# Kernel optimization log

Hardware: AMD Instinct MI355X
Metric: run time of the kernel (lower is better)

Reference implementation:

```python
import jax, jax.numpy as jnp
import numpy as np

VOCAB = 32000
EMBED = 512
CTX = 256
HID = 1024
MAX_SEQ = 1024
B, S = 4, 1024


def setup_inputs() -> dict:
    key = jax.random.key(0)
    ks = jax.random.split(key, 12)
    std = 0.02
    inp = {
        "input_ids": jax.random.randint(ks[0], (B, S), 0, VOCAB, dtype=jnp.int64 if jax.config.jax_enable_x64 else jnp.int32),
        "tok_emb": jax.random.normal(ks[1], (VOCAB, EMBED), jnp.float32) * std,
        "pos_emb": jax.random.normal(ks[2], (MAX_SEQ, EMBED), jnp.float32) * std,
        "W0": jax.random.normal(ks[3], (HID, EMBED + CTX), jnp.float32) * std,
        "b0": jnp.zeros((HID,), jnp.float32),
        "W1": jax.random.normal(ks[4], (HID, HID), jnp.float32) * std,
        "b1": jnp.zeros((HID,), jnp.float32),
        "Wout": jax.random.normal(ks[5], (VOCAB, HID), jnp.float32) * std,
        "bout": jnp.zeros((VOCAB,), jnp.float32),
        "Wc": jax.random.normal(ks[6], (CTX, HID), jnp.float32) * std,
        "bc": jnp.zeros((CTX,), jnp.float32),
    }
    return inp


def reference(input_ids, tok_emb, pos_emb, W0, b0, W1, b1, Wout, bout, Wc, bc):
    # embeddings: [B, S, E]
    seq_len = input_ids.shape[1]
    x = tok_emb[input_ids] + pos_emb[:seq_len][None, :, :]
    ctx0 = jnp.zeros((input_ids.shape[0], Wc.shape[0]), x.dtype)

    def step(ctx, xt):
        # xt: [B, E]; ctx: [B, C]
        h = jax.nn.relu(jnp.concatenate([xt, ctx], axis=-1) @ W0.T + b0)  # layer 0
        h = jax.nn.relu(h @ W1.T + b1)                                    # layer 1
        logits = h @ Wout.T + bout                                        # [B, V]
        new_ctx = ctx + h @ Wc.T + bc
        return new_ctx, (logits, ctx)  # trajectory stores ctx BEFORE update, as in torch

    _, (logits, traj) = jax.lax.scan(step, ctx0, jnp.swapaxes(x, 0, 1))
    # logits: [S, B, V] -> [B, S, V]; traj: [S, B, C] -> [B, S, C]
    return jnp.swapaxes(logits, 0, 1), jnp.swapaxes(traj, 0, 1)
```

## Files before the change

kernel.cpp:

```cpp
#include <hip/hip_runtime.h>
#include <stdint.h>

#define VOCABN 32000
#define EMBEDN 512
#define CTXN   256
#define HIDN   1024
#define BN     4
#define SN     1024
#define MTOT   (BN*SN)

typedef __attribute__((ext_vector_type(8))) short short8;
typedef __attribute__((ext_vector_type(4))) float f32x4;

__device__ __forceinline__ ushort f2bf(float f) {
    uint x = __float_as_uint(f);
    uint r = (x + 0x7FFFu + ((x >> 16) & 1u)) >> 16;
    return (ushort)r;
}
__device__ __forceinline__ float bf2f(ushort h) { return __uint_as_float((uint)h << 16); }
__device__ __forceinline__ float bflo(uint p) { return __uint_as_float(p << 16); }
__device__ __forceinline__ float bfhi(uint p) { return __uint_as_float(p & 0xFFFF0000u); }

__global__ __launch_bounds__(256) void embed_kernel(
    const int* __restrict__ ids, const float* __restrict__ tok,
    const float* __restrict__ pos, ushort* __restrict__ X)
{
    int i = blockIdx.x * 256 + threadIdx.x;
    int m = i >> 7;
    int e4 = (i & 127) * 4;
    int id = ids[m];
    int tp = m & 1023;
    float4 a = *(const float4*)(tok + (size_t)id * EMBEDN + e4);
    float4 b = *(const float4*)(pos + (size_t)tp * EMBEDN + e4);
    ushort4 r;
    r.x = f2bf(a.x + b.x); r.y = f2bf(a.y + b.y);
    r.z = f2bf(a.z + b.z); r.w = f2bf(a.w + b.w);
    *(ushort4*)(X + (size_t)m * EMBEDN + e4) = r;
}

__global__ __launch_bounds__(256) void gemm_bt(
    const ushort* __restrict__ A, const float* __restrict__ B,
    const float* __restrict__ bias, float* __restrict__ C,
    int M, int N, int K, int ldb)
{
    __shared__ ushort As[128 * 40];
    __shared__ ushort Bs[128 * 40];

    const int tid = threadIdx.x;
    const int bm = blockIdx.y, bn = blockIdx.x;
    const int wid = tid >> 6, lane = tid & 63;
    const int wm = wid & 1, wn = wid >> 1;
    const int r15 = lane & 15, kq = lane >> 4;

    f32x4 acc[4][4] = {};

    const int row = tid >> 1, seg = (tid & 1) * 16;
    const ushort* asrc = A + (size_t)(bm * 128 + row) * K + seg;
    const float*  bsrc = B + (size_t)(bn * 128 + row) * ldb + seg;
    ushort* adst = &As[row * 40 + seg];
    ushort* bdst = &Bs[row * 40 + seg];

    for (int k0 = 0; k0 < K; k0 += 32) {
        uint4 a0 = *(const uint4*)(asrc + k0);
        uint4 a1 = *(const uint4*)(asrc + k0 + 8);
        float4 f0 = *(const float4*)(bsrc + k0);
        float4 f1 = *(const float4*)(bsrc + k0 + 4);
        float4 f2 = *(const float4*)(bsrc + k0 + 8);
        float4 f3 = *(const float4*)(bsrc + k0 + 12);
        uint4 p0, p1;
        p0.x = (uint)f2bf(f0.x) | ((uint)f2bf(f0.y) << 16);
        p0.y = (uint)f2bf(f0.z) | ((uint)f2bf(f0.w) << 16);
        p0.z = (uint)f2bf(f1.x) | ((uint)f2bf(f1.y) << 16);
        p0.w = (uint)f2bf(f1.z) | ((uint)f2bf(f1.w) << 16);
        p1.x = (uint)f2bf(f2.x) | ((uint)f2bf(f2.y) << 16);
        p1.y = (uint)f2bf(f2.z) | ((uint)f2bf(f2.w) << 16);
        p1.z = (uint)f2bf(f3.x) | ((uint)f2bf(f3.y) << 16);
        p1.w = (uint)f2bf(f3.z) | ((uint)f2bf(f3.w) << 16);
        *(uint4*)adst = a0;
        *(uint4*)(adst + 8) = a1;
        *(uint4*)bdst = p0;
        *(uint4*)(bdst + 8) = p1;
        __syncthreads();

        short8 af[4], bfv[4];
        #pragma unroll
        for (int mt = 0; mt < 4; ++mt)
            af[mt] = *(const short8*)&As[(wm * 64 + mt * 16 + r15) * 40 + kq * 8];
        #pragma unroll
        for (int nt = 0; nt < 4; ++nt)
            bfv[nt] = *(const short8*)&Bs[(wn * 64 + nt * 16 + r15) * 40 + kq * 8];
        #pragma unroll
        for (int mt = 0; mt < 4; ++mt)
            #pragma unroll
            for (int nt = 0; nt < 4; ++nt)
                acc[mt][nt] = __builtin_amdgcn_mfma_f32_16x16x32_bf16(
                    af[mt], bfv[nt], acc[mt][nt], 0, 0, 0);
        __syncthreads();
    }

    #pragma unroll
    for (int mt = 0; mt < 4; ++mt) {
        #pragma unroll
        for (int nt = 0; nt < 4; ++nt) {
            int n = bn * 128 + wn * 64 + nt * 16 + r15;
            float bv = bias[n];
            #pragma unroll
            for (int i = 0; i < 4; ++i) {
                int m = bm * 128 + wm * 64 + mt * 16 + kq * 4 + i;
                C[(size_t)m * N + n] = acc[mt][nt][i] + bv;
            }
        }
    }
}

__global__ __launch_bounds__(256) void mk_kernel(
    const float* __restrict__ W0, const float* __restrict__ Wc,
    float* __restrict__ M)
{
    __shared__ float w0r[4][256];
    const int tid = threadIdx.x;
    const int i0 = blockIdx.x * 4;
    for (int idx = tid; idx < 1024; idx += 256) {
        int r = idx >> 8, c = idx & 255;
        w0r[r][c] = W0[(size_t)(i0 + r) * 768 + 512 + c];
    }
    __syncthreads();
    for (int rep = 0; rep < 4; ++rep) {
        int j = rep * 256 + tid;
        float a0 = 0, a1 = 0, a2 = 0, a3 = 0;
        for (int c = 0; c < 256; ++c) {
            float wv = Wc[(size_t)c * 1024 + j];
            a0 += w0r[0][c] * wv; a1 += w0r[1][c] * wv;
            a2 += w0r[2][c] * wv; a3 += w0r[3][c] * wv;
        }
        M[(size_t)(i0 + 0) * 1024 + j] = a0;
        M[(size_t)(i0 + 1) * 1024 + j] = a1;
        M[(size_t)(i0 + 2) * 1024 + j] = a2;
        M[(size_t)(i0 + 3) * 1024 + j] = a3;
    }
}

__device__ __forceinline__ void gbar(uint* bar, int& ep) {
    __syncthreads();
    if (threadIdx.x == 0) {
        __hip_atomic_fetch_add(bar, 1u, __ATOMIC_RELEASE, __HIP_MEMORY_SCOPE_AGENT);
        uint tgt = (uint)(++ep) * 64u;
        while (__hip_atomic_load(bar, __ATOMIC_ACQUIRE, __HIP_MEMORY_SCOPE_AGENT) < tgt) {}
    }
    __syncthreads();
}

__global__ __launch_bounds__(256) void rec_kernel(
    const float* __restrict__ W0, const float* __restrict__ W1g,
    const float* __restrict__ b1g, const float* __restrict__ bcg,
    const float* __restrict__ Mg,
    uint* h0hi, uint* h0lo, uint* h1hi, uint* h1lo, uint* bar,
    const float* __restrict__ u_g, ushort* __restrict__ Hout)
{
    extern __shared__ char smem[];
    ushort* W1f_hi = (ushort*)(smem);
    ushort* W1f_lo = (ushort*)(smem + 32768);
    ushort* Mf_hi  = (ushort*)(smem + 65536);
    ushort* Mf_lo  = (ushort*)(smem + 98304);
    uint*   st_hi  = (uint*)(smem + 131072);
    uint*   st_lo  = (uint*)(smem + 139392);
    float*  red    = (float*)(smem + 147712);
    float*  hloc   = (float*)(smem + 148736);
    float*  a_s    = (float*)(smem + 148992);
    float*  b1s    = (float*)(smem + 149248);
    float*  ds_    = (float*)(smem + 149312);

    const int wg = blockIdx.x, tid = threadIdx.x;
    const int wv = tid >> 6, lane = tid & 63;

    for (int idx = tid; idx < 16384; idx += 256) {
        int j = idx & 7, ln = (idx >> 3) & 63, ks = idx >> 9;
        int m = ln & 15, kq = ln >> 4;
        int k = ks * 32 + kq * 8 + j;
        float w1 = W1g[(size_t)(wg * 16 + m) * 1024 + k];
        ushort h = f2bf(w1);
        W1f_hi[idx] = h;
        W1f_lo[idx] = f2bf(w1 - bf2f(h));
        float mm = Mg[(size_t)(wg * 16 + m) * 1024 + k];
        ushort mh = f2bf(mm);
        Mf_hi[idx] = mh;
        Mf_lo[idx] = f2bf(mm - bf2f(mh));
    }
    if (tid < 16) {
        b1s[tid] = b1g[wg * 16 + tid];
        float acc = 0.f;
        for (int c = 0; c < 256; ++c)
            acc += W0[(size_t)(wg * 16 + tid) * 768 + 512 + c] * bcg[c];
        ds_[tid] = acc;
    }
    if (tid < 64) a_s[tid] = 0.f;

    float u_reg = 0.f;
    if (tid < 64)
        u_reg = u_g[(size_t)((tid >> 4) * 1024 + 0) * 1024 + wg * 16 + (tid & 15)];
    __syncthreads();

    int ep = 0;
    for (int t = 0; t < SN; ++t) {
        if (tid < 64) hloc[tid] = fmaxf(u_reg + a_s[tid], 0.f);
        __syncthreads();
        if (tid < 32) {
            int s = tid >> 3, j = tid & 7;
            float x0 = hloc[s * 16 + 2 * j], x1 = hloc[s * 16 + 2 * j + 1];
            ushort p0 = f2bf(x0), p1 = f2bf(x1);
            float r0 = x0 - bf2f(p0), r1 = x1 - bf2f(p1);
            __hip_atomic_store(h0hi + s * 512 + wg * 8 + j,
                (uint)p0 | ((uint)p1 << 16), __ATOMIC_RELAXED, __HIP_MEMORY_SCOPE_AGENT);
            __hip_atomic_store(h0lo + s * 512 + wg * 8 + j,
                (uint)f2bf(r0) | ((uint)f2bf(r1) << 16), __ATOMIC_RELAXED, __HIP_MEMORY_SCOPE_AGENT);
        }
        gbar(bar, ep);

        for (int idx = tid; idx < 2048; idx += 256) {
            int s = idx >> 9, w = idx & 511;
            st_hi[s * 520 + w] = __hip_atomic_load(h0hi + idx, __ATOMIC_RELAXED, __HIP_MEMORY_SCOPE_AGENT);
            st_lo[s * 520 + w] = __hip_atomic_load(h0lo + idx, __ATOMIC_RELAXED, __HIP_MEMORY_SCOPE_AGENT);
        }
        __syncthreads();
        {
            f32x4 acc = {0.f, 0.f, 0.f, 0.f};
            int n = lane & 15, kq = lane >> 4, nc = n & 3;
            #pragma unroll
            for (int s8 = 0; s8 < 8; ++s8) {
                int ks = wv * 8 + s8;
                short8 ah = *(const short8*)&W1f_hi[ks * 512 + lane * 8];
                short8 al = *(const short8*)&W1f_lo[ks * 512 + lane * 8];
                union { uint u[4]; short8 v; } bh, bl;
                #pragma unroll
                for (int q = 0; q < 4; ++q) {
                    bh.u[q] = st_hi[nc * 520 + ks * 16 + kq * 4 + q];
                    bl.u[q] = st_lo[nc * 520 + ks * 16 + kq * 4 + q];
                }
                acc = __builtin_amdgcn_mfma_f32_16x16x32_bf16(ah, bh.v, acc, 0, 0, 0);
                acc = __builtin_amdgcn_mfma_f32_16x16x32_bf16(ah, bl.v, acc, 0, 0, 0);
                acc = __builtin_amdgcn_mfma_f32_16x16x32_bf16(al, bh.v, acc, 0, 0, 0);
            }
            if (n < 4) {
                #pragma unroll
                for (int i = 0; i < 4; ++i) {
                    int m = kq * 4 + i;
                    red[((m * 4 + n) << 2) + wv] = acc[i];
                }
            }
        }
        __syncthreads();
        if (tid < 64) {
            int m = tid >> 2, n = tid & 3;
            const float* rp = &red[(m * 4 + n) << 2];
            float h1 = fmaxf(rp[0] + rp[1] + rp[2] + rp[3] + b1s[m], 0.f);
            hloc[n * 16 + m] = h1;
            Hout[(size_t)(n * 1024 + t) * 1024 + wg * 16 + m] = f2bf(h1);
        }
        __syncthreads();
        if (tid < 32) {
            int s = tid >> 3, j = tid & 7;
            float x0 = hloc[s * 16 + 2 * j], x1 = hloc[s * 16 + 2 * j + 1];
            ushort p0 = f2bf(x0), p1 = f2bf(x1);
            float r0 = x0 - bf2f(p0), r1 = x1 - bf2f(p1);
            __hip_atomic_store(h1hi + s * 512 + wg * 8 + j,
                (uint)p0 | ((uint)p1 << 16), __ATOMIC_RELAXED, __HIP_MEMORY_SCOPE_AGENT);
            __hip_atomic_store(h1lo + s * 512 + wg * 8 + j,
                (uint)f2bf(r0) | ((uint)f2bf(r1) << 16), __ATOMIC_RELAXED, __HIP_MEMORY_SCOPE_AGENT);
        }
        gbar(bar, ep);

        for (int idx = tid; idx < 2048; idx += 256) {
            int s = idx >> 9, w = idx & 511;
            st_hi[s * 520 + w] = __hip_atomic_load(h1hi + idx, __ATOMIC_RELAXED, __HIP_MEMORY_SCOPE_AGENT);
            st_lo[s * 520 + w] = __hip_atomic_load(h1lo + idx, __ATOMIC_RELAXED, __HIP_MEMORY_SCOPE_AGENT);
        }
        if (tid < 64) {
            int tn = (t < 1023) ? t + 1 : 1023;
            u_reg = u_g[(size_t)((tid >> 4) * 1024 + tn) * 1024 + wg * 16 + (tid & 15)];
        }
        __syncthreads();
        {
            f32x4 acc = {0.f, 0.f, 0.f, 0.f};
            int n = lane & 15, kq = lane >> 4, nc = n & 3;
            #pragma unroll
            for (int s8 = 0; s8 < 8; ++s8) {
                int ks = wv * 8 + s8;
                short8 ah = *(const short8*)&Mf_hi[ks * 512 + lane * 8];
                short8 al = *(const short8*)&Mf_lo[ks * 512 + lane * 8];
                union { uint u[4]; short8 v; } bh, bl;
                #pragma unroll
                for (int q = 0; q < 4; ++q) {
                    bh.u[q] = st_hi[nc * 520 + ks * 16 + kq * 4 + q];
                    bl.u[q] = st_lo[nc * 520 + ks * 16 + kq * 4 + q];
                }
                acc = __builtin_amdgcn_mfma_f32_16x16x32_bf16(ah, bh.v, acc, 0, 0, 0);
                acc = __builtin_amdgcn_mfma_f32_16x16x32_bf16(ah, bl.v, acc, 0, 0, 0);
                acc = __builtin_amdgcn_mfma_f32_16x16x32_bf16(al, bh.v, acc, 0, 0, 0);
            }
            if (n < 4) {
                #pragma unroll
                for (int i = 0; i < 4; ++i) {
                    int m = kq * 4 + i;
                    red[((m * 4 + n) << 2) + wv] = acc[i];
                }
            }
        }
        __syncthreads();
        if (tid < 64) {
            int m = tid >> 2, n = tid & 3;
            const float* rp = &red[(m * 4 + n) << 2];
            a_s[n * 16 + m] += rp[0] + rp[1] + rp[2] + rp[3] + ds_[m];
        }
        __syncthreads();
    }
}

__global__ __launch_bounds__(256) void scan_kernel(
    const float* __restrict__ P, float* __restrict__ traj)
{
    __shared__ float lds[32][257];
    const int b = blockIdx.x, tid = threadIdx.x;
    float carry = 0.f;
    for (int tt = 0; tt < 32; ++tt) {
        int t0 = tt * 32;
        for (int idx = tid; idx < 32 * 256; idx += 256) {
            int i = idx >> 8, c = idx & 255;
            lds[i][c] = P[(size_t)(b * 1024 + t0 + i) * 256 + c];
        }
        __syncthreads();
        #pragma unroll 1
        for (int i = 0; i < 32; ++i) {
            float old = carry;
            carry += lds[i][tid];
            lds[i][tid] = old;
        }
        __syncthreads();
        for (int idx = tid; idx < 32 * 256; idx += 256) {
            int i = idx >> 8, c = idx & 255;
            traj[(size_t)(b * 1024 + t0 + i) * 256 + c] = lds[i][c];
        }
        __syncthreads();
    }
}

extern "C" void kernel_launch(void* const* d_in, const int* in_sizes, int n_in,
                              void* d_out, int out_size, void* d_ws, size_t ws_size,
                              hipStream_t stream)
{
    const int*   ids  = (const int*)d_in[0];
    const float* tok  = (const float*)d_in[1];
    const float* pos  = (const float*)d_in[2];
    const float* W0   = (const float*)d_in[3];
    const float* b0   = (const float*)d_in[4];
    const float* W1   = (const float*)d_in[5];
    const float* b1   = (const float*)d_in[6];
    const float* Wout = (const float*)d_in[7];
    const float* bout = (const float*)d_in[8];
    const float* Wc   = (const float*)d_in[9];
    const float* bc   = (const float*)d_in[10];
    float* out = (float*)d_out;
    char* ws = (char*)d_ws;

    uint*   h0hi = (uint*)(ws + 0);
    uint*   h0lo = (uint*)(ws + 8192);
    uint*   h1hi = (uint*)(ws + 16384);
    uint*   h1lo = (uint*)(ws + 24576);
    uint*   bar  = (uint*)(ws + 32768);
    float*  Mg   = (float*)(ws + 65536);
    float*  u_g  = (float*)(ws + 65536 + 4194304);
    ushort* Hbuf = (ushort*)(ws + 65536 + 4194304 + 16777216);
    ushort* Xbuf = (ushort*)(ws + 65536 + 4194304 + 16777216 + 8388608);
    float*  Pbuf = (float*)(ws + 65536 + 4194304 + 16777216 + 8388608 + 4194304);

    hipMemsetAsync(ws, 0, 36864, stream);

    hipFuncSetAttribute(reinterpret_cast<const void*>(rec_kernel),
                        hipFuncAttributeMaxDynamicSharedMemorySize, 149376);

    embed_kernel<<<2048, 256, 0, stream>>>(ids, tok, pos, Xbuf);

    gemm_bt<<<dim3(8, 32), 256, 0, stream>>>(Xbuf, W0, b0, u_g,
                                             MTOT, HIDN, EMBEDN, 768);

    mk_kernel<<<256, 256, 0, stream>>>(W0, Wc, Mg);

    rec_kernel<<<64, 256, 149376, stream>>>(W0, W1, b1, bc, Mg,
                                            h0hi, h0lo, h1hi, h1lo, bar,
                                            u_g, Hbuf);

    gemm_bt<<<dim3(250, 32), 256, 0, stream>>>(Hbuf, Wout, bout, out,
                                               MTOT, VOCABN, HIDN, HIDN);

    gemm_bt<<<dim3(2, 32), 256, 0, stream>>>(Hbuf, Wc, bc, Pbuf,
                                             MTOT, CTXN, HIDN, HIDN);
    scan_kernel<<<4, 256, 0, stream>>>(Pbuf, out + (size_t)131072000);
}
```

Baseline: 16.04 ms.

## Replace atomic-counter grid barrier with per-block flag publishing and wavefront polling

Swaps the central fetch-add grid barrier in the recurrent kernel for per-workgroup monotonic flags. Each block publishes its flag with a release store, and one wavefront polls all 64 flags in parallel before an acquire fence. Hi/lo bf16 halves are packed into a single 32-bit publish word and read back as 64-bit loads, and per-thread state moves from LDS into registers, which removes several __syncthreads per step. The goal is lower latency per serial timestep. The cost is extra polling traffic, and correctness now depends on the release/acquire ordering being right.

```diff
diff --git a/kernel.cpp b/kernel.cpp
--- a/kernel.cpp
+++ b/kernel.cpp
@@ -11,6 +11,7 @@
 
 typedef __attribute__((ext_vector_type(8))) short short8;
 typedef __attribute__((ext_vector_type(4))) float f32x4;
+typedef unsigned long long u64;
 
 __device__ __forceinline__ ushort f2bf(float f) {
     uint x = __float_as_uint(f);
@@ -18,8 +19,6 @@
     return (ushort)r;
 }
 __device__ __forceinline__ float bf2f(ushort h) { return __uint_as_float((uint)h << 16); }
-__device__ __forceinline__ float bflo(uint p) { return __uint_as_float(p << 16); }
-__device__ __forceinline__ float bfhi(uint p) { return __uint_as_float(p & 0xFFFF0000u); }
 
 __global__ __launch_bounds__(256) void embed_kernel(
     const int* __restrict__ ids, const float* __restrict__ tok,
@@ -140,12 +139,14 @@
     }
 }
 
-__device__ __forceinline__ void gbar(uint* bar, int& ep) {
-    __syncthreads();
-    if (threadIdx.x == 0) {
-        __hip_atomic_fetch_add(bar, 1u, __ATOMIC_RELEASE, __HIP_MEMORY_SCOPE_AGENT);
-        uint tgt = (uint)(++ep) * 64u;
-        while (__hip_atomic_load(bar, __ATOMIC_ACQUIRE, __HIP_MEMORY_SCOPE_AGENT) < tgt) {}
+__device__ __forceinline__ void wait_flags(uint* flags, uint target) {
+    if (threadIdx.x < 64) {
+        uint v;
+        do {
+            v = __hip_atomic_load(flags + threadIdx.x, __ATOMIC_RELAXED,
+                                  __HIP_MEMORY_SCOPE_AGENT);
+        } while (__any(v < target));
+        __builtin_amdgcn_fence(__ATOMIC_ACQUIRE, "agent");
     }
     __syncthreads();
 }
@@ -154,7 +155,7 @@
     const float* __restrict__ W0, const float* __restrict__ W1g,
     const float* __restrict__ b1g, const float* __restrict__ bcg,
     const float* __restrict__ Mg,
-    uint* h0hi, uint* h0lo, uint* h1hi, uint* h1lo, uint* bar,
+    uint* pub0, uint* pub1, uint* flag0, uint* flag1,
     const float* __restrict__ u_g, ushort* __restrict__ Hout)
 {
     extern __shared__ char smem[];
@@ -165,10 +166,6 @@
     uint*   st_hi  = (uint*)(smem + 131072);
     uint*   st_lo  = (uint*)(smem + 139392);
     float*  red    = (float*)(smem + 147712);
-    float*  hloc   = (float*)(smem + 148736);
-    float*  a_s    = (float*)(smem + 148992);
-    float*  b1s    = (float*)(smem + 149248);
-    float*  ds_    = (float*)(smem + 149312);
 
     const int wg = blockIdx.x, tid = threadIdx.x;
     const int wv = tid >> 6, lane = tid & 63;
@@ -186,40 +183,46 @@
         Mf_hi[idx] = mh;
         Mf_lo[idx] = f2bf(mm - bf2f(mh));
     }
-    if (tid < 16) {
-        b1s[tid] = b1g[wg * 16 + tid];
+
+    float a_reg = 0.f, u_reg = 0.f, b1_reg = 0.f, ds_reg = 0.f;
+    if (tid < 64) {
+        int m = tid & 15, n = tid >> 4;
+        b1_reg = b1g[wg * 16 + m];
         float acc = 0.f;
         for (int c = 0; c < 256; ++c)
-            acc += W0[(size_t)(wg * 16 + tid) * 768 + 512 + c] * bcg[c];
-        ds_[tid] = acc;
-    }
-    if (tid < 64) a_s[tid] = 0.f;
-
-    float u_reg = 0.f;
-    if (tid < 64)
-        u_reg = u_g[(size_t)((tid >> 4) * 1024 + 0) * 1024 + wg * 16 + (tid & 15)];
+            acc += W0[(size_t)(wg * 16 + m) * 768 + 512 + c] * bcg[c];
+        ds_reg = acc;
+        u_reg = u_g[(size_t)(n * 1024 + 0) * 1024 + wg * 16 + m];
+    }
     __syncthreads();
 
-    int ep = 0;
     for (int t = 0; t < SN; ++t) {
-        if (tid < 64) hloc[tid] = fmaxf(u_reg + a_s[tid], 0.f);
-        __syncthreads();
-        if (tid < 32) {
-            int s = tid >> 3, j = tid & 7;
-            float x0 = hloc[s * 16 + 2 * j], x1 = hloc[s * 16 + 2 * j + 1];
-            ushort p0 = f2bf(x0), p1 = f2bf(x1);
-            float r0 = x0 - bf2f(p0), r1 = x1 - bf2f(p1);
-            __hip_atomic_store(h0hi + s * 512 + wg * 8 + j,
-                (uint)p0 | ((uint)p1 << 16), __ATOMIC_RELAXED, __HIP_MEMORY_SCOPE_AGENT);
-            __hip_atomic_store(h0lo + s * 512 + wg * 8 + j,
-                (uint)f2bf(r0) | ((uint)f2bf(r1) << 16), __ATOMIC_RELAXED, __HIP_MEMORY_SCOPE_AGENT);
-        }
-        gbar(bar, ep);
-
-        for (int idx = tid; idx < 2048; idx += 256) {
-            int s = idx >> 9, w = idx & 511;
-            st_hi[s * 520 + w] = __hip_atomic_load(h0hi + idx, __ATOMIC_RELAXED, __HIP_MEMORY_SCOPE_AGENT);
-            st_lo[s * 520 + w] = __hip_atomic_load(h0lo + idx, __ATOMIC_RELAXED, __HIP_MEMORY_SCOPE_AGENT);
+        const uint tgt = (uint)(t + 1);
+
+        if (tid < 64) {
+            int m = tid & 15, n = tid >> 4;
+            float x = fmaxf(u_reg + a_reg, 0.f);
+            ushort ph = f2bf(x);
+            uint w = (uint)ph | ((uint)f2bf(x - bf2f(ph)) << 16);
+            __hip_atomic_store(pub0 + n * 1024 + wg * 16 + m, w,
+                               __ATOMIC_RELAXED, __HIP_MEMORY_SCOPE_AGENT);
+            if (tid == 0)
+                __hip_atomic_store(flag0 + wg, tgt,
+                                   __ATOMIC_RELEASE, __HIP_MEMORY_SCOPE_AGENT);
+        }
+        wait_flags(flag0, tgt);
+
+        {
+            const u64* p64 = (const u64*)pub0;
+            #pragma unroll
+            for (int idx = tid; idx < 2048; idx += 256) {
+                u64 v = __hip_atomic_load(p64 + idx, __ATOMIC_RELAXED,
+                                          __HIP_MEMORY_SCOPE_AGENT);
+                uint v0 = (uint)v, v1 = (uint)(v >> 32);
+                int s = idx >> 9, w = idx & 511;
+                st_hi[s * 520 + w] = (v0 & 0xFFFFu) | (v1 << 16);
+                st_lo[s * 520 + w] = (v0 >> 16) | (v1 & 0xFFFF0000u);
+            }
         }
         __syncthreads();
         {
@@ -250,33 +253,36 @@
         }
         __syncthreads();
         if (tid < 64) {
-            int m = tid >> 2, n = tid & 3;
-            const float* rp = &red[(m * 4 + n) << 2];
-            float h1 = fmaxf(rp[0] + rp[1] + rp[2] + rp[3] + b1s[m], 0.f);
-            hloc[n * 16 + m] = h1;
+            int m = tid & 15, n = tid >> 4;
+            f32x4 r4 = *(const f32x4*)&red[(m * 4 + n) << 2];
+            float h1 = fmaxf(r4[0] + r4[1] + r4[2] + r4[3] + b1_reg, 0.f);
             Hout[(size_t)(n * 1024 + t) * 1024 + wg * 16 + m] = f2bf(h1);
-        }
-        __syncthreads();
-        if (tid < 32) {
-            int s = tid >> 3, j = tid & 7;
-            float x0 = hloc[s * 16 + 2 * j], x1 = hloc[s * 16 + 2 * j + 1];
-            ushort p0 = f2bf(x0), p1 = f2bf(x1);
-            float r0 = x0 - bf2f(p0), r1 = x1 - bf2f(p1);
-            __hip_atomic_store(h1hi + s * 512 + wg * 8 + j,
-                (uint)p0 | ((uint)p1 << 16), __ATOMIC_RELAXED, __HIP_MEMORY_SCOPE_AGENT);
-            __hip_atomic_store(h1lo + s * 512 + wg * 8 + j,
-                (uint)f2bf(r0) | ((uint)f2bf(r1) << 16), __ATOMIC_RELAXED, __HIP_MEMORY_SCOPE_AGENT);
-        }
-        gbar(bar, ep);
-
-        for (int idx = tid; idx < 2048; idx += 256) {
-            int s = idx >> 9, w = idx & 511;
-            st_hi[s * 520 + w] = __hip_atomic_load(h1hi + idx, __ATOMIC_RELAXED, __HIP_MEMORY_SCOPE_AGENT);
-            st_lo[s * 520 + w] = __hip_atomic_load(h1lo + idx, __ATOMIC_RELAXED, __HIP_MEMORY_SCOPE_AGENT);
+            ushort ph = f2bf(h1);
+            uint w = (uint)ph | ((uint)f2bf(h1 - bf2f(ph)) << 16);
+            __hip_atomic_store(pub1 + n * 1024 + wg * 16 + m, w,
+                               __ATOMIC_RELAXED, __HIP_MEMORY_SCOPE_AGENT);
+            if (tid == 0)
+                __hip_atomic_store(flag1 + wg, tgt,
+                                   __ATOMIC_RELEASE, __HIP_MEMORY_SCOPE_AGENT);
+        }
+        wait_flags(flag1, tgt);
+
+        {
+            const u64* p64 = (const u64*)pub1;
+            #pragma unroll
+            for (int idx = tid; idx < 2048; idx += 256) {
+                u64 v = __hip_atomic_load(p64 + idx, __ATOMIC_RELAXED,
+                                          __HIP_MEMORY_SCOPE_AGENT);
+                uint v0 = (uint)v, v1 = (uint)(v >> 32);
+                int s = idx >> 9, w = idx & 511;
+                st_hi[s * 520 + w] = (v0 & 0xFFFFu) | (v1 << 16);
+                st_lo[s * 520 + w] = (v0 >> 16) | (v1 & 0xFFFF0000u);
+            }
         }
         if (tid < 64) {
+            int m = tid & 15, n = tid >> 4;
             int tn = (t < 1023) ? t + 1 : 1023;
-            u_reg = u_g[(size_t)((tid >> 4) * 1024 + tn) * 1024 + wg * 16 + (tid & 15)];
+            u_reg = u_g[(size_t)(n * 1024 + tn) * 1024 + wg * 16 + m];
         }
         __syncthreads();
         {
@@ -307,11 +313,10 @@
         }
         __syncthreads();
         if (tid < 64) {
-            int m = tid >> 2, n = tid & 3;
-            const float* rp = &red[(m * 4 + n) << 2];
-            a_s[n * 16 + m] += rp[0] + rp[1] + rp[2] + rp[3] + ds_[m];
-        }
-        __syncthreads();
+            int m = tid & 15, n = tid >> 4;
+            f32x4 r4 = *(const f32x4*)&red[(m * 4 + n) << 2];
+            a_reg += r4[0] + r4[1] + r4[2] + r4[3] + ds_reg;
+        }
     }
 }
 
@@ -361,11 +366,10 @@
     float* out = (float*)d_out;
     char* ws = (char*)d_ws;
 
-    uint*   h0hi = (uint*)(ws + 0);
-    uint*   h0lo = (uint*)(ws + 8192);
-    uint*   h1hi = (uint*)(ws + 16384);
-    uint*   h1lo = (uint*)(ws + 24576);
-    uint*   bar  = (uint*)(ws + 32768);
+    uint*   pub0  = (uint*)(ws + 0);
+    uint*   pub1  = (uint*)(ws + 16384);
+    uint*   flag0 = (uint*)(ws + 32768);
+    uint*   flag1 = (uint*)(ws + 33024);
     float*  Mg   = (float*)(ws + 65536);
     float*  u_g  = (float*)(ws + 65536 + 4194304);
     ushort* Hbuf = (ushort*)(ws + 65536 + 4194304 + 16777216);
@@ -375,7 +379,7 @@
     hipMemsetAsync(ws, 0, 36864, stream);
 
     hipFuncSetAttribute(reinterpret_cast<const void*>(rec_kernel),
-                        hipFuncAttributeMaxDynamicSharedMemorySize, 149376);
+                        hipFuncAttributeMaxDynamicSharedMemorySize, 148736);
 
     embed_kernel<<<2048, 256, 0, stream>>>(ids, tok, pos, Xbuf);
 
@@ -384,8 +388,8 @@
 
     mk_kernel<<<256, 256, 0, stream>>>(W0, Wc, Mg);
 
-    rec_kernel<<<64, 256, 149376, stream>>>(W0, W1, b1, bc, Mg,
-                                            h0hi, h0lo, h1hi, h1lo, bar,
+    rec_kernel<<<64, 256, 148736, stream>>>(W0, W1, b1, bc, Mg,
+                                            pub0, pub1, flag0, flag1,
                                             u_g, Hbuf);
 
     gemm_bt<<<dim3(250, 32), 256, 0, stream>>>(Hbuf, Wout, bout, out,
```

New measurement: 13.63 ms. -15.1%, faster.
